# Performance work log

Hardware: AMD Instinct MI355X
Metric: run time of the kernel (lower is better)

The kernel has to match this reference:

```python
import jax, jax.numpy as jnp
import numpy as np

EPS = 1e-5  # nn.BatchNorm2d default eps
K = 3       # number of adjacency subsets


def setup_inputs() -> dict:
    key = jax.random.key(0)
    ks = jax.random.split(key, 8)
    N, C, T, V = 64, 64, 256, 25
    Cout = 64
    x = jax.random.normal(ks[0], (N, C, T, V), dtype=jnp.float32)
    A = jax.random.uniform(ks[1], (K, V, V), dtype=jnp.float32) * 0.1  # normalized-ish adjacency
    PA = jnp.ones((K, V, V), dtype=jnp.float32)  # torch.ones_like(A) init
    Wc = jax.random.normal(ks[2], (K * Cout, C), dtype=jnp.float32) * 0.05  # 1x1 conv weight
    bc = jax.random.normal(ks[3], (K * Cout,), dtype=jnp.float32) * 0.01
    gamma = 0.5 + jax.random.uniform(ks[4], (Cout,), dtype=jnp.float32)
    beta = jax.random.normal(ks[5], (Cout,), dtype=jnp.float32) * 0.1
    mean = jax.random.normal(ks[6], (Cout,), dtype=jnp.float32) * 0.1
    var = 0.5 + jax.random.uniform(ks[7], (Cout,), dtype=jnp.float32)
    return {"x": x, "A": A, "PA": PA, "Wc": Wc, "bc": bc,
            "gamma": gamma, "beta": beta, "mean": mean, "var": var}


def reference(x, A, PA, Wc, bc, gamma, beta, mean, var):
    # x: (n, c, t, v). in_channels == out_channels -> residual is identity.
    n, c, t, v = x.shape
    res = x
    Aeff = A * PA  # (k, v, w)
    # 1x1 conv: (n,c,t,v) x (o,c) -> (n,o,t,v), o = K*Cout
    y = jnp.einsum('nctv,oc->notv', x, Wc) + bc[None, :, None, None]
    cout = y.shape[1] // K
    y = y.reshape(n, K, cout, t, v)
    # per-subset graph aggregation: (n,k,c,t,v) x (k,v,w) -> (n,c,t,w)
    z = jnp.einsum('nkctv,kvw->nctw', y, Aeff)
    # BatchNorm2d (eval mode) over channel dim
    inv = jax.lax.rsqrt(var + EPS)
    bn = (z - mean[None, :, None, None]) * (gamma * inv)[None, :, None, None] + beta[None, :, None, None]
    return jax.nn.relu(bn + res)
```

## Files before the change

kernel.cpp:

```cpp
#include <hip/hip_runtime.h>
#include <hip/hip_bf16.h>

typedef __attribute__((ext_vector_type(8))) short short8;
typedef __attribute__((ext_vector_type(4))) float floatx4;

#define TT 8
#define XS_PITCH 264
#define KCP 200

__device__ __forceinline__ float bf2f(unsigned short u) {
    unsigned int xx = ((unsigned int)u) << 16;
    return __uint_as_float(xx);
}
__device__ __forceinline__ unsigned short f2bf(float f) {
    unsigned int xx = __float_as_uint(f);
    unsigned int r = (xx + 0x7fffu + ((xx >> 16) & 1u)) >> 16;
    return (unsigned short)r;
}

__global__ __launch_bounds__(512) void gcn_fused(
    const float* __restrict__ x,  const float* __restrict__ A,
    const float* __restrict__ PA, const float* __restrict__ Wc,
    const float* __restrict__ bc, const float* __restrict__ gamma_,
    const float* __restrict__ beta_, const float* __restrict__ mean_,
    const float* __restrict__ var_, float* __restrict__ out)
{
#if defined(__gfx950__)
    __shared__ __align__(16) unsigned short Xs[64 * XS_PITCH];
    __shared__ __align__(16) unsigned short AsL[96 * 32];
    __shared__ __align__(16) unsigned short XAs[32 * KCP];
    __shared__ float colsumL[96];
    __shared__ float sL[64], b2L[64], bcL[192];

    const int tid = threadIdx.x;
    const int n  = blockIdx.x >> 5;
    const int t0 = (blockIdx.x & 31) * TT;

    const float* xn = x + (size_t)n * 64 * 256 * 25;
    for (int idx = tid; idx < 64 * TT * 32; idx += 512) {
        int c = idx >> 8, r = idx & 255;
        int t = r >> 5, v = r & 31;
        float val = 0.f;
        if (v < 25) val = xn[(c * 256 + t0 + t) * 25 + v];
        Xs[c * XS_PITCH + r] = f2bf(val);
    }
    for (int idx = tid; idx < 96 * 32; idx += 512) {
        int kw = idx >> 5, v = idx & 31;
        int k = kw >> 5, w = kw & 31;
        unsigned short val = 0;
        if (w < 25 && v < 25) {
            int ai = (k * 25 + v) * 25 + w;
            val = f2bf(A[ai] * PA[ai]);
        }
        AsL[kw * 32 + v] = val;
    }
    if (tid < 96) {
        int k = tid >> 5, w = tid & 31;
        float s = 0.f;
        if (w < 25)
            for (int v = 0; v < 25; ++v) {
                int ai = (k * 25 + v) * 25 + w;
                s += A[ai] * PA[ai];
            }
        colsumL[tid] = s;
    }
    if (tid < 64) {
        float sc = gamma_[tid] * rsqrtf(var_[tid] + 1e-5f);
        sL[tid]  = sc;
        b2L[tid] = beta_[tid] - mean_[tid] * sc;
    }
    if (tid < 192) bcL[tid] = bc[tid];
    __syncthreads();

    const int wave = tid >> 6, lane = tid & 63;
    const int l15 = lane & 15, quad = lane >> 4;

    const int ntA = wave & 3, wmA = wave >> 2;
    short8 aA[3];
#pragma unroll
    for (int ii = 0; ii < 3; ++ii) {
        int mt = wmA + 2 * ii;
        aA[ii] = *(const short8*)&AsL[(mt * 16 + l15) * 32 + quad * 8];
    }

    const int cot = wave & 3, wt = wave >> 2;
    union U8 { short8 v; unsigned short s[8]; };
    short8 wf[6];
#pragma unroll
    for (int ks = 0; ks < 6; ++ks) {
        int k = ks >> 1;
        int co = cot * 16 + l15;
        int cpart = (ks & 1) * 32 + quad * 8;
        const float* wp = &Wc[(k * 64 + co) * 64 + cpart];
        U8 u;
#pragma unroll
        for (int j = 0; j < 8; ++j) u.s[j] = f2bf(wp[j]);
        wf[ks] = u.v;
    }

    for (int t = 0; t < TT; ++t) {
        short8 xb = *(const short8*)&Xs[(ntA * 16 + l15) * XS_PITCH + t * 32 + quad * 8];
        floatx4 fr[3];
#pragma unroll
        for (int ii = 0; ii < 3; ++ii) {
            floatx4 z0 = {0.f, 0.f, 0.f, 0.f};
            fr[ii] = __builtin_amdgcn_mfma_f32_16x16x32_bf16(aA[ii], xb, z0, 0, 0, 0);
        }
        __syncthreads();
#pragma unroll
        for (int ii = 0; ii < 3; ++ii) {
            int mt = wmA + 2 * ii;
#pragma unroll
            for (int r = 0; r < 4; ++r) {
                int kw = mt * 16 + quad * 4 + r;
                int w = kw & 31, k = kw >> 5;
                XAs[w * KCP + k * 64 + ntA * 16 + l15] = f2bf(fr[ii][r]);
            }
        }
        __syncthreads();

        floatx4 zacc = {0.f, 0.f, 0.f, 0.f};
        const unsigned short* xr = &XAs[(wt * 16 + l15) * KCP];
#pragma unroll
        for (int ks = 0; ks < 6; ++ks) {
            short8 bfr = *(const short8*)&xr[ks * 32 + quad * 8];
            zacc = __builtin_amdgcn_mfma_f32_16x16x32_bf16(wf[ks], bfr, zacc, 0, 0, 0);
        }

        int w = wt * 16 + l15;
        if (w < 25) {
            float cs0 = colsumL[w], cs1 = colsumL[32 + w], cs2 = colsumL[64 + w];
#pragma unroll
            for (int r = 0; r < 4; ++r) {
                int co = cot * 16 + quad * 4 + r;
                float bterm = bcL[co] * cs0 + bcL[64 + co] * cs1 + bcL[128 + co] * cs2;
                float xres = bf2f(Xs[co * XS_PITCH + t * 32 + w]);
                float val = sL[co] * (zacc[r] + bterm) + b2L[co] + xres;
                out[((size_t)(n * 64 + co) * 256 + t0 + t) * 25 + w] = fmaxf(val, 0.f);
            }
        }
    }
#else
    (void)x; (void)A; (void)PA; (void)Wc; (void)bc;
    (void)gamma_; (void)beta_; (void)mean_; (void)var_; (void)out;
#endif
}

extern "C" void kernel_launch(void* const* d_in, const int* in_sizes, int n_in,
                              void* d_out, int out_size, void* d_ws, size_t ws_size,
                              hipStream_t stream) {
    (void)in_sizes; (void)n_in; (void)d_ws; (void)ws_size; (void)out_size;
    gcn_fused<<<dim3(64 * 32), dim3(512), 0, stream>>>(
        (const float*)d_in[0],
        (const float*)d_in[1],
        (const float*)d_in[2],
        (const float*)d_in[3],
        (const float*)d_in[4],
        (const float*)d_in[5],
        (const float*)d_in[6],
        (const float*)d_in[7],
        (const float*)d_in[8],
        (float*)d_out);
}
```

Measured before the change: 306.3 us.

## Split weight prep into a separate kernel and restructure main GCN kernel per-wave

A small prep kernel now converts Wc, A*PA, the folded bias/BN shift and the BN scale into a workspace once per call, so each main block no longer redoes that setup. The main kernel uses 256-thread blocks over 4 time steps with one wave per time step. Each wave computes x·Aeff first into a private swizzled LDS buffer and then applies the channel weights, with no block-wide barriers inside the loop. It also adds vectorized loads of x and reads weights directly from global or L2 per MFMA, which trades register-held weights for extra memory traffic and adds a second kernel launch.

```diff
diff --git a/kernel.cpp b/kernel.cpp
--- a/kernel.cpp
+++ b/kernel.cpp
@@ -3,162 +3,212 @@
 
 typedef __attribute__((ext_vector_type(8))) short short8;
 typedef __attribute__((ext_vector_type(4))) float floatx4;
-
-#define TT 8
-#define XS_PITCH 264
-#define KCP 200
+typedef __attribute__((ext_vector_type(4))) unsigned short ushortx4;
+
+#define TT 4
+#define XS_PITCH 136
+
+#define WS_W2 0
+#define WS_AE 24576
+#define WS_F  30720
+#define WS_S  38912
 
 __device__ __forceinline__ float bf2f(unsigned short u) {
-    unsigned int xx = ((unsigned int)u) << 16;
-    return __uint_as_float(xx);
+    return __uint_as_float(((unsigned int)u) << 16);
 }
 __device__ __forceinline__ unsigned short f2bf(float f) {
     unsigned int xx = __float_as_uint(f);
-    unsigned int r = (xx + 0x7fffu + ((xx >> 16) & 1u)) >> 16;
-    return (unsigned short)r;
-}
-
-__global__ __launch_bounds__(512) void gcn_fused(
-    const float* __restrict__ x,  const float* __restrict__ A,
-    const float* __restrict__ PA, const float* __restrict__ Wc,
-    const float* __restrict__ bc, const float* __restrict__ gamma_,
-    const float* __restrict__ beta_, const float* __restrict__ mean_,
-    const float* __restrict__ var_, float* __restrict__ out)
+    return (unsigned short)((xx + 0x7fffu + ((xx >> 16) & 1u)) >> 16);
+}
+
+__global__ __launch_bounds__(256) void gcn_prep(
+    const float* __restrict__ A, const float* __restrict__ PA,
+    const float* __restrict__ Wc, const float* __restrict__ bc,
+    const float* __restrict__ gamma_, const float* __restrict__ beta_,
+    const float* __restrict__ mean_, const float* __restrict__ var_,
+    unsigned short* __restrict__ w2, unsigned short* __restrict__ ae,
+    float* __restrict__ Fx, float* __restrict__ sarr)
+{
+    const int b = blockIdx.x, tid = threadIdx.x;
+    if (b == 0) {
+        __shared__ float cs[96];
+        if (tid < 96) {
+            int k = tid >> 5, w = tid & 31;
+            float s = 0.f;
+            if (w < 25)
+                for (int v = 0; v < 25; ++v) {
+                    int ai = (k * 25 + v) * 25 + w;
+                    s += A[ai] * PA[ai];
+                }
+            cs[tid] = s;
+        }
+        if (tid < 64) sarr[tid] = gamma_[tid] * rsqrtf(var_[tid] + 1e-5f);
+        __syncthreads();
+        for (int e = tid; e < 2048; e += 256) {
+            int w = e >> 6, co = e & 63;
+            float val = 0.f;
+            if (w < 25) {
+                float sc = gamma_[co] * rsqrtf(var_[co] + 1e-5f);
+                val = beta_[co] - mean_[co] * sc
+                    + sc * (bc[co] * cs[w] + bc[64 + co] * cs[32 + w] + bc[128 + co] * cs[64 + w]);
+            }
+            Fx[e] = val;
+        }
+    } else if (b == 1) {
+        for (int e = tid; e < 3072; e += 256) {
+            int k = e >> 10, r = e & 1023, w = r >> 5, v = r & 31;
+            unsigned short val = 0;
+            if (v < 25 && w < 25) {
+                int ai = (k * 25 + v) * 25 + w;
+                val = f2bf(A[ai] * PA[ai]);
+            }
+            ae[e] = val;
+        }
+    } else {
+        const int half = b - 2;
+        for (int e = tid + half * 6144; e < (half + 1) * 6144; e += 256) {
+            int co = e / 192, kc = e % 192, k = kc >> 6, c = kc & 63;
+            w2[e] = f2bf(Wc[(k * 64 + co) * 64 + c]);
+        }
+    }
+}
+
+__global__ __launch_bounds__(256, 4) void gcn_main(
+    const float* __restrict__ x,
+    const unsigned short* __restrict__ w2g,
+    const unsigned short* __restrict__ aeg,
+    const float* __restrict__ Fg,
+    const float* __restrict__ sg,
+    float* __restrict__ out)
 {
 #if defined(__gfx950__)
     __shared__ __align__(16) unsigned short Xs[64 * XS_PITCH];
-    __shared__ __align__(16) unsigned short AsL[96 * 32];
-    __shared__ __align__(16) unsigned short XAs[32 * KCP];
-    __shared__ float colsumL[96];
-    __shared__ float sL[64], b2L[64], bcL[192];
+    __shared__ __align__(16) unsigned short XAbuf[4 * 2 * 1024];
 
     const int tid = threadIdx.x;
-    const int n  = blockIdx.x >> 5;
-    const int t0 = (blockIdx.x & 31) * TT;
-
-    const float* xn = x + (size_t)n * 64 * 256 * 25;
-    for (int idx = tid; idx < 64 * TT * 32; idx += 512) {
-        int c = idx >> 8, r = idx & 255;
-        int t = r >> 5, v = r & 31;
-        float val = 0.f;
-        if (v < 25) val = xn[(c * 256 + t0 + t) * 25 + v];
-        Xs[c * XS_PITCH + r] = f2bf(val);
-    }
-    for (int idx = tid; idx < 96 * 32; idx += 512) {
-        int kw = idx >> 5, v = idx & 31;
-        int k = kw >> 5, w = kw & 31;
-        unsigned short val = 0;
-        if (w < 25 && v < 25) {
-            int ai = (k * 25 + v) * 25 + w;
-            val = f2bf(A[ai] * PA[ai]);
-        }
-        AsL[kw * 32 + v] = val;
-    }
-    if (tid < 96) {
-        int k = tid >> 5, w = tid & 31;
-        float s = 0.f;
-        if (w < 25)
-            for (int v = 0; v < 25; ++v) {
-                int ai = (k * 25 + v) * 25 + w;
-                s += A[ai] * PA[ai];
-            }
-        colsumL[tid] = s;
-    }
-    if (tid < 64) {
-        float sc = gamma_[tid] * rsqrtf(var_[tid] + 1e-5f);
-        sL[tid]  = sc;
-        b2L[tid] = beta_[tid] - mean_[tid] * sc;
-    }
-    if (tid < 192) bcL[tid] = bc[tid];
-    __syncthreads();
+    const int n  = blockIdx.x >> 6;
+    const int t0 = (blockIdx.x & 63) * TT;
+    const float* xn = x + (size_t)n * 409600;
+
+    {
+        const int c = tid >> 2, tl = tid & 3;
+        const float* gp = xn + (c * 256 + t0 + tl) * 25;
+        unsigned short* dst = &Xs[c * XS_PITCH + tl * 32];
+        float f[32];
+#pragma unroll
+        for (int j = 0; j < 25; ++j) f[j] = gp[j];
+#pragma unroll
+        for (int j = 25; j < 32; ++j) f[j] = 0.f;
+#pragma unroll
+        for (int vc = 0; vc < 4; ++vc) {
+            union { short8 v; unsigned short s[8]; } u;
+#pragma unroll
+            for (int j = 0; j < 8; ++j) u.s[j] = f2bf(f[vc * 8 + j]);
+            *(short8*)&dst[vc * 8] = u.v;
+        }
+    }
 
     const int wave = tid >> 6, lane = tid & 63;
     const int l15 = lane & 15, quad = lane >> 4;
-
-    const int ntA = wave & 3, wmA = wave >> 2;
-    short8 aA[3];
-#pragma unroll
-    for (int ii = 0; ii < 3; ++ii) {
-        int mt = wmA + 2 * ii;
-        aA[ii] = *(const short8*)&AsL[(mt * 16 + l15) * 32 + quad * 8];
-    }
-
-    const int cot = wave & 3, wt = wave >> 2;
-    union U8 { short8 v; unsigned short s[8]; };
-    short8 wf[6];
-#pragma unroll
-    for (int ks = 0; ks < 6; ++ks) {
-        int k = ks >> 1;
-        int co = cot * 16 + l15;
-        int cpart = (ks & 1) * 32 + quad * 8;
-        const float* wp = &Wc[(k * 64 + co) * 64 + cpart];
-        U8 u;
-#pragma unroll
-        for (int j = 0; j < 8; ++j) u.s[j] = f2bf(wp[j]);
-        wf[ks] = u.v;
-    }
-
-    for (int t = 0; t < TT; ++t) {
-        short8 xb = *(const short8*)&Xs[(ntA * 16 + l15) * XS_PITCH + t * 32 + quad * 8];
-        floatx4 fr[3];
-#pragma unroll
-        for (int ii = 0; ii < 3; ++ii) {
-            floatx4 z0 = {0.f, 0.f, 0.f, 0.f};
-            fr[ii] = __builtin_amdgcn_mfma_f32_16x16x32_bf16(aA[ii], xb, z0, 0, 0, 0);
-        }
-        __syncthreads();
-#pragma unroll
-        for (int ii = 0; ii < 3; ++ii) {
-            int mt = wmA + 2 * ii;
-#pragma unroll
-            for (int r = 0; r < 4; ++r) {
-                int kw = mt * 16 + quad * 4 + r;
-                int w = kw & 31, k = kw >> 5;
-                XAs[w * KCP + k * 64 + ntA * 16 + l15] = f2bf(fr[ii][r]);
+    const int t = wave;
+
+    short8 aeffB[3][2];
+#pragma unroll
+    for (int k = 0; k < 3; ++k)
+#pragma unroll
+        for (int nt = 0; nt < 2; ++nt)
+            aeffB[k][nt] = *(const short8*)&aeg[(k * 32 + nt * 16 + l15) * 32 + quad * 8];
+
+    __syncthreads();
+
+    unsigned short* xa = &XAbuf[wave * 2048];
+    const int wlo3 = l15 & 3, qh = quad >> 1, ql = quad & 1;
+    const int woff00 = (l15     ) * 64 + (((0 + qh) ^ wlo3) << 4) + ql * 8;
+    const int woff01 = (16 + l15) * 64 + (((0 + qh) ^ wlo3) << 4) + ql * 8;
+    const int woff10 = (l15     ) * 64 + (((2 + qh) ^ wlo3) << 4) + ql * 8;
+    const int woff11 = (16 + l15) * 64 + (((2 + qh) ^ wlo3) << 4) + ql * 8;
+    const int roff0  = (l15     ) * 64 + ((quad ^ wlo3) << 4);
+    const int roff1  = (16 + l15) * 64 + ((quad ^ wlo3) << 4);
+
+    const floatx4 zero4 = {0.f, 0.f, 0.f, 0.f};
+    floatx4 zacc[4][2];
+#pragma unroll
+    for (int ct = 0; ct < 4; ++ct) { zacc[ct][0] = zero4; zacc[ct][1] = zero4; }
+
+    const unsigned short* xsrow = &Xs[t * 32 + quad * 8];
+
+#pragma unroll
+    for (int ch = 0; ch < 6; ++ch) {
+        const int k = ch >> 1, cc = ch & 1;
+        char* xab = (char*)xa + (ch & 1) * 2048;
+
+        short8 xf0 = *(const short8*)&xsrow[(cc * 32      + l15) * XS_PITCH];
+        short8 xf1 = *(const short8*)&xsrow[(cc * 32 + 16 + l15) * XS_PITCH];
+        floatx4 d00 = __builtin_amdgcn_mfma_f32_16x16x32_bf16(xf0, aeffB[k][0], zero4, 0, 0, 0);
+        floatx4 d01 = __builtin_amdgcn_mfma_f32_16x16x32_bf16(xf0, aeffB[k][1], zero4, 0, 0, 0);
+        floatx4 d10 = __builtin_amdgcn_mfma_f32_16x16x32_bf16(xf1, aeffB[k][0], zero4, 0, 0, 0);
+        floatx4 d11 = __builtin_amdgcn_mfma_f32_16x16x32_bf16(xf1, aeffB[k][1], zero4, 0, 0, 0);
+
+        {
+            ushortx4 p;
+            p[0] = f2bf(d00[0]); p[1] = f2bf(d00[1]); p[2] = f2bf(d00[2]); p[3] = f2bf(d00[3]);
+            *(ushortx4*)(xab + woff00) = p;
+            p[0] = f2bf(d01[0]); p[1] = f2bf(d01[1]); p[2] = f2bf(d01[2]); p[3] = f2bf(d01[3]);
+            *(ushortx4*)(xab + woff01) = p;
+            p[0] = f2bf(d10[0]); p[1] = f2bf(d10[1]); p[2] = f2bf(d10[2]); p[3] = f2bf(d10[3]);
+            *(ushortx4*)(xab + woff10) = p;
+            p[0] = f2bf(d11[0]); p[1] = f2bf(d11[1]); p[2] = f2bf(d11[2]); p[3] = f2bf(d11[3]);
+            *(ushortx4*)(xab + woff11) = p;
+        }
+
+        short8 b0 = *(const short8*)(xab + roff0);
+        short8 b1 = *(const short8*)(xab + roff1);
+        const unsigned short* wrow = &w2g[l15 * 192 + k * 64 + cc * 32 + quad * 8];
+#pragma unroll
+        for (int ct = 0; ct < 4; ++ct) {
+            short8 wf = *(const short8*)&wrow[ct * 16 * 192];
+            zacc[ct][0] = __builtin_amdgcn_mfma_f32_16x16x32_bf16(wf, b0, zacc[ct][0], 0, 0, 0);
+            zacc[ct][1] = __builtin_amdgcn_mfma_f32_16x16x32_bf16(wf, b1, zacc[ct][1], 0, 0, 0);
+        }
+    }
+
+    const unsigned short* resp = &Xs[(quad * 4) * XS_PITCH + t * 32 + l15];
+    float* outp = out + ((size_t)(n * 64 + quad * 4) * 256 + t0 + t) * 25 + l15;
+#pragma unroll
+    for (int ct = 0; ct < 4; ++ct) {
+        floatx4 sv = *(const floatx4*)&sg[ct * 16 + quad * 4];
+#pragma unroll
+        for (int wt = 0; wt < 2; ++wt) {
+            floatx4 Fv = *(const floatx4*)&Fg[(wt * 16 + l15) * 64 + ct * 16 + quad * 4];
+            if (wt == 0 || l15 < 9) {
+#pragma unroll
+                for (int r = 0; r < 4; ++r) {
+                    float xres = bf2f(resp[(ct * 16 + r) * XS_PITCH + wt * 16]);
+                    float val = sv[r] * zacc[ct][wt][r] + Fv[r] + xres;
+                    outp[(size_t)(ct * 16 + r) * 6400 + wt * 16] = fmaxf(val, 0.f);
+                }
             }
         }
-        __syncthreads();
-
-        floatx4 zacc = {0.f, 0.f, 0.f, 0.f};
-        const unsigned short* xr = &XAs[(wt * 16 + l15) * KCP];
-#pragma unroll
-        for (int ks = 0; ks < 6; ++ks) {
-            short8 bfr = *(const short8*)&xr[ks * 32 + quad * 8];
-            zacc = __builtin_amdgcn_mfma_f32_16x16x32_bf16(wf[ks], bfr, zacc, 0, 0, 0);
-        }
-
-        int w = wt * 16 + l15;
-        if (w < 25) {
-            float cs0 = colsumL[w], cs1 = colsumL[32 + w], cs2 = colsumL[64 + w];
-#pragma unroll
-            for (int r = 0; r < 4; ++r) {
-                int co = cot * 16 + quad * 4 + r;
-                float bterm = bcL[co] * cs0 + bcL[64 + co] * cs1 + bcL[128 + co] * cs2;
-                float xres = bf2f(Xs[co * XS_PITCH + t * 32 + w]);
-                float val = sL[co] * (zacc[r] + bterm) + b2L[co] + xres;
-                out[((size_t)(n * 64 + co) * 256 + t0 + t) * 25 + w] = fmaxf(val, 0.f);
-            }
-        }
     }
 #else
-    (void)x; (void)A; (void)PA; (void)Wc; (void)bc;
-    (void)gamma_; (void)beta_; (void)mean_; (void)var_; (void)out;
+    (void)x; (void)w2g; (void)aeg; (void)Fg; (void)sg; (void)out;
 #endif
 }
 
 extern "C" void kernel_launch(void* const* d_in, const int* in_sizes, int n_in,
                               void* d_out, int out_size, void* d_ws, size_t ws_size,
                               hipStream_t stream) {
-    (void)in_sizes; (void)n_in; (void)d_ws; (void)ws_size; (void)out_size;
-    gcn_fused<<<dim3(64 * 32), dim3(512), 0, stream>>>(
-        (const float*)d_in[0],
-        (const float*)d_in[1],
-        (const float*)d_in[2],
-        (const float*)d_in[3],
-        (const float*)d_in[4],
-        (const float*)d_in[5],
-        (const float*)d_in[6],
-        (const float*)d_in[7],
-        (const float*)d_in[8],
-        (float*)d_out);
-}
+    (void)in_sizes; (void)n_in; (void)out_size; (void)ws_size;
+    unsigned short* w2 = (unsigned short*)((char*)d_ws + WS_W2);
+    unsigned short* ae = (unsigned short*)((char*)d_ws + WS_AE);
+    float*          Fx = (float*)((char*)d_ws + WS_F);
+    float*          sa = (float*)((char*)d_ws + WS_S);
+
+    gcn_prep<<<dim3(4), dim3(256), 0, stream>>>(
+        (const float*)d_in[1], (const float*)d_in[2], (const float*)d_in[3],
+        (const float*)d_in[4], (const float*)d_in[5], (const float*)d_in[6],
+        (const float*)d_in[7], (const float*)d_in[8], w2, ae, Fx, sa);
+
+    gcn_main<<<dim3(64 * 64), dim3(256), 0, stream>>>(
+        (const float*)d_in[0], w2, ae, Fx, sa, (float*)d_out);
+}
```

Measured after the change: 270.8 us. -11.6%, faster.
